# Performance work log

Hardware: AMD Instinct MI355X
Metric: run time of the kernel (lower is better)

The kernel has to match this reference:

```python
import jax, jax.numpy as jnp
from jax import lax
import numpy as np

Z, Y, X = 224, 512, 512
P = 15                      # prediction_bands
W_DIM = P + 4               # max(P+3, 4+P)
DYN = 16
MAX_VAL = 2.0 ** (DYN - 1) - 1.0
MIN_VAL = -(2.0 ** (DYN - 1))
V_MIN = 4.0
V_MAX = 6.0
ALPHA = 0.1


def setup_inputs() -> dict:
    key = jax.random.key(0)
    image = jax.random.normal(key, (Z, Y, X), dtype=jnp.float32)
    weights = jnp.zeros((Z, W_DIM), dtype=jnp.float32)      # register_buffer 'weights'
    local_sums = jnp.zeros((Z, 4), dtype=jnp.float32)       # register_buffer 'local_sums'
    return {"image": image, "weights": weights, "local_sums": local_sums}


def reference(image, weights, local_sums):
    # sample_representatives = image.clone(); never modified in the visible code path
    reps = image
    # front-pad with P zero bands so that padded[z : z+P] == bands z-P .. z-1 (zero-padded)
    padded_spec = jnp.concatenate(
        [jnp.zeros((P, Y, X), image.dtype), reps], axis=0)

    def band_step(carry, z):
        w_all, ls_all = carry
        rep_z = reps[z]                                   # [Y, X]
        pad = jnp.pad(rep_z, 1)                            # zero pad, matches F.pad(...,0)
        north = pad[:-2, 1:-1]
        west = pad[1:-1, :-2]
        nw = pad[:-2, :-2]
        fourth = (north + west + nw) / 3.0
        spatial = jnp.stack([north, west, nw, fourth], axis=-1)        # [Y,X,4]
        spec = lax.dynamic_slice_in_dim(padded_spec, z, P, axis=0)     # [P,Y,X]
        spec = jnp.moveaxis(spec, 0, -1)                               # [Y,X,P]
        predictors = jnp.concatenate([spatial, spec], axis=-1)        # [Y,X,P+4] == W_DIM

        w_row = w_all[z]                                   # [W_DIM]
        pred = jnp.einsum('yxc,c->yx', predictors, w_row)
        pred = jnp.clip(pred, MIN_VAL, MAX_VAL)
        resid = image[z] - pred

        # local differences (CCSDS directional differences)
        d1 = north - west
        d2 = west - nw
        d3 = nw - north
        d4 = north + west - 2.0 * nw
        mld = jnp.stack([d1.mean(), d2.mean(), d3.mean(), d4.mean()])  # [4]
        mean_res = resid.mean()

        # weight adaptation (spatial components)
        abs_d = jnp.abs(mld)
        V_i = jnp.where(abs_d >= 1.0,
                        jnp.floor(jnp.log2(jnp.maximum(abs_d, 1e-30))),
                        0.0)
        damping = 2.0 ** (-jnp.maximum(0.0, V_i - V_MAX))
        upd = (2.0 ** (-V_MIN)) * mean_res * mld * damping
        upd = jnp.where(abs_d > 1e-8, upd, 0.0)
        w_new = w_row.at[:4].add(upd)
        # spectral components: indices 4 .. 4+P
        w_new = w_new.at[4:4 + P].add((2.0 ** (-V_MIN)) * mean_res * 0.1)
        w_new = jnp.clip(w_new, -2.0, 2.0)
        w_all = w_all.at[z].set(w_new)
        ls_all = ls_all.at[z].set((1.0 - ALPHA) * ls_all[z] + ALPHA * mld)
        return (w_all, ls_all), (pred, resid)

    (_, _), (preds, resids) = lax.scan(band_step, (weights, local_sums),
                                       jnp.arange(Z))
    return preds, resids
```

## Files before the change

kernel.cpp:

```cpp
#include <hip/hip_runtime.h>

constexpr int Zd = 224;
constexpr int Yd = 512;
constexpr int Xd = 512;
constexpr int Pd = 15;
constexpr int WDIM = Pd + 4;
constexpr float MAXV = 32767.0f;
constexpr float MINV = -32768.0f;

__global__ __launch_bounds__(256) void spec_pred_kernel(
    const float* __restrict__ image,
    const float* __restrict__ weights,
    float* __restrict__ preds,
    float* __restrict__ resids)
{
    const int z = blockIdx.z;
    const int y = blockIdx.y * blockDim.y + threadIdx.y;
    const int x = threadIdx.x * 4;

    const long long YX = (long long)Yd * Xd;
    const long long rowoff = (long long)z * YX + (long long)y * Xd;
    const float* row = image + rowoff;

    const float* wr = weights + z * WDIM;
    const float w3 = wr[3] * (1.0f / 3.0f);
    const float cn  = wr[0] + w3;
    const float cw  = wr[1] + w3;
    const float cnw = wr[2] + w3;

    const float4 self = *(const float4*)(row + x);
    float4 north = make_float4(0.f, 0.f, 0.f, 0.f);
    float sleft = 0.f, nleft = 0.f;
    if (y > 0) {
        const float* nrow = row - Xd;
        north = *(const float4*)(nrow + x);
        if (x > 0) nleft = nrow[x - 1];
    }
    if (x > 0) sleft = row[x - 1];

    const float4 west = make_float4(sleft, self.x, self.y, self.z);
    const float4 nwv  = make_float4(nleft, north.x, north.y, north.z);

    float p0 = cn * north.x + cw * west.x + cnw * nwv.x;
    float p1 = cn * north.y + cw * west.y + cnw * nwv.y;
    float p2 = cn * north.z + cw * west.z + cnw * nwv.z;
    float p3 = cn * north.w + cw * west.w + cnw * nwv.w;

#pragma unroll
    for (int k = 0; k < Pd; ++k) {
        const int zk = z - Pd + k;
        if (zk >= 0) {
            const float4 s = *(const float4*)(image + (long long)zk * YX +
                                              (long long)y * Xd + x);
            const float wk = wr[4 + k];
            p0 = fmaf(wk, s.x, p0);
            p1 = fmaf(wk, s.y, p1);
            p2 = fmaf(wk, s.z, p2);
            p3 = fmaf(wk, s.w, p3);
        }
    }

    p0 = fminf(fmaxf(p0, MINV), MAXV);
    p1 = fminf(fmaxf(p1, MINV), MAXV);
    p2 = fminf(fmaxf(p2, MINV), MAXV);
    p3 = fminf(fmaxf(p3, MINV), MAXV);

    const float4 pv = make_float4(p0, p1, p2, p3);
    const float4 rv = make_float4(self.x - p0, self.y - p1,
                                  self.z - p2, self.w - p3);
    *(float4*)(preds  + rowoff + x) = pv;
    *(float4*)(resids + rowoff + x) = rv;
}

extern "C" void kernel_launch(void* const* d_in, const int* in_sizes, int n_in,
                              void* d_out, int out_size, void* d_ws, size_t ws_size,
                              hipStream_t stream) {
    const float* image   = (const float*)d_in[0];
    const float* weights = (const float*)d_in[1];

    float* preds  = (float*)d_out;
    float* resids = (float*)d_out + (long long)Zd * Yd * Xd;

    dim3 block(128, 2, 1);
    dim3 grid(1, Yd / 2, Zd);
    spec_pred_kernel<<<grid, block, 0, stream>>>(image, weights, preds, resids);
}
```

Before: 736.3 us.

## Roll spectral history in registers across z chunks instead of reloading bands

Each thread now walks a chunk of 56 bands along z, keeping the previous 15 bands for its 4 pixels in a register ring buffer. This removes the 15 redundant spectral loads per output. In exchange the grid shrinks to 1024 blocks with a serial z loop, reducing parallelism and latency hiding, and register pressure rises.

```diff
diff --git a/kernel.cpp b/kernel.cpp
--- a/kernel.cpp
+++ b/kernel.cpp
@@ -8,68 +8,83 @@
 constexpr float MAXV = 32767.0f;
 constexpr float MINV = -32768.0f;
 
-__global__ __launch_bounds__(256) void spec_pred_kernel(
+constexpr int NCHUNK = 4;
+constexpr int CHUNK  = Zd / NCHUNK;
+
+__global__ __launch_bounds__(256, 4) void spec_pred_roll(
     const float* __restrict__ image,
     const float* __restrict__ weights,
     float* __restrict__ preds,
     float* __restrict__ resids)
 {
-    const int z = blockIdx.z;
-    const int y = blockIdx.y * blockDim.y + threadIdx.y;
-    const int x = threadIdx.x * 4;
+    const int y  = blockIdx.y * 2 + threadIdx.y;
+    const int x  = threadIdx.x * 4;
+    const int z0 = blockIdx.x * CHUNK;
 
-    const long long YX = (long long)Yd * Xd;
-    const long long rowoff = (long long)z * YX + (long long)y * Xd;
-    const float* row = image + rowoff;
+    const long long YX  = (long long)Yd * Xd;
+    const long long yx  = (long long)y * Xd + x;
 
-    const float* wr = weights + z * WDIM;
-    const float w3 = wr[3] * (1.0f / 3.0f);
-    const float cn  = wr[0] + w3;
-    const float cw  = wr[1] + w3;
-    const float cnw = wr[2] + w3;
+    float4 h[Pd];
+#pragma unroll
+    for (int k = 0; k < Pd; ++k) {
+        const int zk = z0 - Pd + k;
+        h[k] = (zk >= 0) ? *(const float4*)(image + (long long)zk * YX + yx)
+                         : make_float4(0.f, 0.f, 0.f, 0.f);
+    }
 
-    const float4 self = *(const float4*)(row + x);
-    float4 north = make_float4(0.f, 0.f, 0.f, 0.f);
-    float sleft = 0.f, nleft = 0.f;
-    if (y > 0) {
-        const float* nrow = row - Xd;
-        north = *(const float4*)(nrow + x);
-        if (x > 0) nleft = nrow[x - 1];
-    }
-    if (x > 0) sleft = row[x - 1];
+    const float* row0 = image + yx;
 
-    const float4 west = make_float4(sleft, self.x, self.y, self.z);
-    const float4 nwv  = make_float4(nleft, north.x, north.y, north.z);
+    for (int i = 0; i < CHUNK; ++i) {
+        const int z = z0 + i;
+        const float* row = row0 + (long long)z * YX;
 
-    float p0 = cn * north.x + cw * west.x + cnw * nwv.x;
-    float p1 = cn * north.y + cw * west.y + cnw * nwv.y;
-    float p2 = cn * north.z + cw * west.z + cnw * nwv.z;
-    float p3 = cn * north.w + cw * west.w + cnw * nwv.w;
+        const float* wr = weights + z * WDIM;
+        const float w3  = wr[3] * (1.0f / 3.0f);
+        const float cn  = wr[0] + w3;
+        const float cw  = wr[1] + w3;
+        const float cnw = wr[2] + w3;
+
+        const float4 self = *(const float4*)(row);
+        float4 north = make_float4(0.f, 0.f, 0.f, 0.f);
+        float sleft = 0.f, nleft = 0.f;
+        if (y > 0) {
+            const float* nrow = row - Xd;
+            north = *(const float4*)(nrow);
+            if (x > 0) nleft = nrow[-1];
+        }
+        if (x > 0) sleft = row[-1];
+
+        const float4 west = make_float4(sleft, self.x, self.y, self.z);
+        const float4 nwv  = make_float4(nleft, north.x, north.y, north.z);
+
+        float p0 = cn * north.x + cw * west.x + cnw * nwv.x;
+        float p1 = cn * north.y + cw * west.y + cnw * nwv.y;
+        float p2 = cn * north.z + cw * west.z + cnw * nwv.z;
+        float p3 = cn * north.w + cw * west.w + cnw * nwv.w;
 
 #pragma unroll
-    for (int k = 0; k < Pd; ++k) {
-        const int zk = z - Pd + k;
-        if (zk >= 0) {
-            const float4 s = *(const float4*)(image + (long long)zk * YX +
-                                              (long long)y * Xd + x);
+        for (int k = 0; k < Pd; ++k) {
             const float wk = wr[4 + k];
-            p0 = fmaf(wk, s.x, p0);
-            p1 = fmaf(wk, s.y, p1);
-            p2 = fmaf(wk, s.z, p2);
-            p3 = fmaf(wk, s.w, p3);
+            p0 = fmaf(wk, h[k].x, p0);
+            p1 = fmaf(wk, h[k].y, p1);
+            p2 = fmaf(wk, h[k].z, p2);
+            p3 = fmaf(wk, h[k].w, p3);
         }
+
+        p0 = fminf(fmaxf(p0, MINV), MAXV);
+        p1 = fminf(fmaxf(p1, MINV), MAXV);
+        p2 = fminf(fmaxf(p2, MINV), MAXV);
+        p3 = fminf(fmaxf(p3, MINV), MAXV);
+
+        const long long o = (long long)z * YX + yx;
+        *(float4*)(preds  + o) = make_float4(p0, p1, p2, p3);
+        *(float4*)(resids + o) = make_float4(self.x - p0, self.y - p1,
+                                             self.z - p2, self.w - p3);
+
+#pragma unroll
+        for (int k = 0; k < Pd - 1; ++k) h[k] = h[k + 1];
+        h[Pd - 1] = self;
     }
-
-    p0 = fminf(fmaxf(p0, MINV), MAXV);
-    p1 = fminf(fmaxf(p1, MINV), MAXV);
-    p2 = fminf(fmaxf(p2, MINV), MAXV);
-    p3 = fminf(fmaxf(p3, MINV), MAXV);
-
-    const float4 pv = make_float4(p0, p1, p2, p3);
-    const float4 rv = make_float4(self.x - p0, self.y - p1,
-                                  self.z - p2, self.w - p3);
-    *(float4*)(preds  + rowoff + x) = pv;
-    *(float4*)(resids + rowoff + x) = rv;
 }
 
 extern "C" void kernel_launch(void* const* d_in, const int* in_sizes, int n_in,
@@ -82,6 +97,6 @@
     float* resids = (float*)d_out + (long long)Zd * Yd * Xd;
 
     dim3 block(128, 2, 1);
-    dim3 grid(1, Yd / 2, Zd);
-    spec_pred_kernel<<<grid, block, 0, stream>>>(image, weights, preds, resids);
+    dim3 grid(NCHUNK, Yd / 2, 1);
+    spec_pred_roll<<<grid, block, 0, stream>>>(image, weights, preds, resids);
 }
```

New measurement: 626.4 us. -14.9%, faster.
